# Performance work log

Hardware: AMD Instinct MI355X
Metric: run time of the kernel (lower is better)

## Reference

```python
import jax, jax.numpy as jnp
import numpy as np
import math

B, T, D, H = 4, 2048, 1024, 16
DH = D // H

def setup_inputs() -> dict:
    key = jax.random.key(0)
    ks = jax.random.split(key, 12)
    s = 1.0 / math.sqrt(D)
    inp = {
        'q': jax.random.normal(ks[0], (B, T, D), jnp.float32),
        'k': jax.random.normal(ks[1], (B, T, D), jnp.float32),
        'v': jax.random.normal(ks[2], (B, T, D), jnp.float32),
        # causal attn_mask [B, Tq, Tk]; all-keep padding mask [B,1,1,Tk]
        'attn_mask': jnp.broadcast_to(jnp.tril(jnp.ones((T, T), jnp.bool_)), (B, T, T)),
        'key_keep_mask': jnp.ones((B, 1, 1, T), jnp.bool_),
        'wq_w': jax.random.normal(ks[3], (D, D), jnp.float32) * s,
        'wq_b': jnp.zeros((D,), jnp.float32),
        'wk_w': jax.random.normal(ks[4], (D, D), jnp.float32) * s,
        'wk_b': jnp.zeros((D,), jnp.float32),
        'wv_w': jax.random.normal(ks[5], (D, D), jnp.float32) * s,
        'wv_b': jnp.zeros((D,), jnp.float32),
        'wo_w': jax.random.normal(ks[6], (D, D), jnp.float32) * s,
        'wo_b': jnp.zeros((D,), jnp.float32),
    }
    return inp

def reference(q, k, v, attn_mask, key_keep_mask, wq_w, wq_b, wk_w, wk_b, wv_w, wv_b, wo_w, wo_b):
    # projections (torch Linear: x @ W^T + b)
    Q = (q @ wq_w.T + wq_b).reshape(B, -1, H, DH).transpose(0, 2, 1, 3)  # [B,H,Tq,DH]
    K = (k @ wk_w.T + wk_b).reshape(B, -1, H, DH).transpose(0, 2, 1, 3)
    V = (v @ wv_w.T + wv_b).reshape(B, -1, H, DH).transpose(0, 2, 1, 3)
    scores = jnp.einsum('bhqd,bhkd->bhqk', Q, K) / math.sqrt(DH)
    neg_inf = jnp.array(-jnp.inf, scores.dtype)
    scores = jnp.where(attn_mask[:, None, :, :], scores, neg_inf)
    scores = jnp.where(key_keep_mask, scores, neg_inf)
    attn = jax.nn.softmax(scores, axis=-1)  # dropout p=0 -> identity
    out = jnp.einsum('bhqk,bhkd->bhqd', attn, V)
    out = out.transpose(0, 2, 1, 3).reshape(B, -1, D)
    return out @ wo_w.T + wo_b
```

## Files before the change

kernel.cpp:

```cpp
#include <hip/hip_runtime.h>
#include <cstdint>
#include <cstddef>


typedef float f32x4 __attribute__((ext_vector_type(4)));
typedef short bf16x8 __attribute__((ext_vector_type(8)));
typedef float fltx4 __attribute__((ext_vector_type(4)));
typedef unsigned short u16x4 __attribute__((ext_vector_type(4)));

#define GLOBAL_AS __attribute__((address_space(1)))
#define LDS_AS __attribute__((address_space(3)))

__device__ __forceinline__ unsigned short f2bf(float f) {
    union { float f; unsigned int u; } x;
    x.f = f;
    unsigned int u = x.u;
    unsigned int r = (u + 0x7FFFu + ((u >> 16) & 1u)) >> 16;
    return (unsigned short)r;
}

__device__ __forceinline__ unsigned int pack_trunc(float a, float b) {
    union { float f; unsigned int u; } x, y;
    x.f = a; y.f = b;
    return (x.u >> 16) | (y.u & 0xFFFF0000u);
}

__global__ __launch_bounds__(256) void cast_all_kernel(
    const float* __restrict__ q, const float* __restrict__ k, const float* __restrict__ v,
    const float* __restrict__ wq, const float* __restrict__ wk,
    const float* __restrict__ wv, const float* __restrict__ wo,
    unsigned short* __restrict__ dst)
{
    const size_t SEG = 8388608;
    const size_t WSEG = 1048576;
    size_t i = ((size_t)blockIdx.x * 256 + threadIdx.x) * 4;
    const float* src;
    size_t off;
    if (i < SEG)               { src = q;  off = i; }
    else if (i < 2 * SEG)      { src = k;  off = i - SEG; }
    else if (i < 3 * SEG)      { src = v;  off = i - 2 * SEG; }
    else if (i < 3 * SEG + WSEG)     { src = wq; off = i - 3 * SEG; }
    else if (i < 3 * SEG + 2 * WSEG) { src = wk; off = i - 3 * SEG - WSEG; }
    else if (i < 3 * SEG + 3 * WSEG) { src = wv; off = i - 3 * SEG - 2 * WSEG; }
    else                             { src = wo; off = i - 3 * SEG - 3 * WSEG; }
    fltx4 val = *(const fltx4*)(src + off);
    u16x4 o;
    o[0] = f2bf(val[0]);
    o[1] = f2bf(val[1]);
    o[2] = f2bf(val[2]);
    o[3] = f2bf(val[3]);
    *(u16x4*)(dst + i) = o;
}

__global__ __launch_bounds__(256) void qkv_gemm_kernel(
    const unsigned short* __restrict__ X,
    const unsigned short* __restrict__ Wc,
    const float* __restrict__ bq, const float* __restrict__ bk,
    const float* __restrict__ bv,
    unsigned short* __restrict__ Outs,
    float qscale)
{
    const int z = blockIdx.z;
    const unsigned short* A  = X  + (size_t)z * 8388608;
    const unsigned short* Bw = Wc + (size_t)z * 1048576;
    const float* bias = (z == 0) ? bq : (z == 1) ? bk : bv;
    unsigned short* outp = Outs + (size_t)z * 8388608;
    const float scale = (z == 0) ? qscale : 1.0f;
    const bool vmode = (z == 2);

    __shared__ __align__(16) unsigned short lA[128 * 32];
    __shared__ __align__(16) unsigned short lB[128 * 32];
    const int tid = threadIdx.x;
    const int w = tid >> 6, lane = tid & 63;
    const int quad = lane >> 4, l16 = lane & 15;

    const int lin = blockIdx.x + (blockIdx.y << 3);
    const int r_ = lin & 7, s_ = lin >> 3;
    const int bm = ((r_ << 3) | (s_ & 7)) * 128;
    const int bn = (s_ >> 3) * 128;

    const int wm = (w >> 1) * 64, wn = (w & 1) * 64;

    f32x4 acc[4][4] = {};
    const int srow0 = w * 16 + (lane >> 2);

    for (int kb = 0; kb < 32; ++kb) {
        const unsigned short* Ab = A + (size_t)bm * 1024 + kb * 32;
        const unsigned short* Bb = Bw + (size_t)bn * 1024 + kb * 32;
#pragma unroll
        for (int i = 0; i < 2; ++i) {
            int row = i * 64 + srow0;
            int gcb = (lane & 3) ^ ((row >> 1) & 3);
            __builtin_amdgcn_global_load_lds(
                (const GLOBAL_AS unsigned int*)(Ab + (size_t)row * 1024 + gcb * 8),
                (LDS_AS unsigned int*)(lA + i * 2048 + w * 512), 16, 0, 0);
            __builtin_amdgcn_global_load_lds(
                (const GLOBAL_AS unsigned int*)(Bb + (size_t)row * 1024 + gcb * 8),
                (LDS_AS unsigned int*)(lB + i * 2048 + w * 512), 16, 0, 0);
        }
        __syncthreads();

        bf16x8 af[4], bfr[4];
#pragma unroll
        for (int mi = 0; mi < 4; ++mi) {
            int row = wm + mi * 16 + l16;
            af[mi] = *(const bf16x8*)(lA + row * 32 + ((quad ^ ((row >> 1) & 3)) * 8));
        }
#pragma unroll
        for (int ni = 0; ni < 4; ++ni) {
            int row = wn + ni * 16 + l16;
            bfr[ni] = *(const bf16x8*)(lB + row * 32 + ((quad ^ ((row >> 1) & 3)) * 8));
        }
#pragma unroll
        for (int mi = 0; mi < 4; ++mi)
#pragma unroll
            for (int ni = 0; ni < 4; ++ni)
                acc[mi][ni] = __builtin_amdgcn_mfma_f32_16x16x32_bf16(af[mi], bfr[ni], acc[mi][ni], 0, 0, 0);
        __syncthreads();
    }

#pragma unroll
    for (int mi = 0; mi < 4; ++mi) {
        int rowb = bm + wm + mi * 16 + quad * 4;
#pragma unroll
        for (int ni = 0; ni < 4; ++ni) {
            int col = bn + wn + ni * 16 + l16;
            float bv_ = bias[col];
#pragma unroll
            for (int r = 0; r < 4; ++r) {
                int m = rowb + r;
                float vout = (acc[mi][ni][r] + bv_) * scale;
                int b = m >> 11, t = m & 2047, h = col >> 6, d = col & 63;
                if (!vmode) {
                    outp[((size_t)(b * 16 + h) * 2048 + t) * 64 + d] = f2bf(vout);
                } else {
                    outp[((size_t)(b * 16 + h) * 64 + d) * 2048 + t] = f2bf(vout);
                }
            }
        }
    }
}

__global__ __launch_bounds__(256) void out_gemm_kernel(
    const unsigned short* __restrict__ A,
    const unsigned short* __restrict__ Bw,
    const float* __restrict__ bias,
    float* __restrict__ outp)
{
    __shared__ __align__(16) unsigned short lA[128 * 32];
    __shared__ __align__(16) unsigned short lB[128 * 32];
    const int tid = threadIdx.x;
    const int w = tid >> 6, lane = tid & 63;
    const int quad = lane >> 4, l16 = lane & 15;

    const int lin = blockIdx.x + (blockIdx.y << 3);
    const int r_ = lin & 7, s_ = lin >> 3;
    const int bm = ((r_ << 3) | (s_ & 7)) * 128;
    const int bn = (s_ >> 3) * 128;

    const int wm = (w >> 1) * 64, wn = (w & 1) * 64;

    f32x4 acc[4][4] = {};
    const int srow0 = w * 16 + (lane >> 2);

    for (int kb = 0; kb < 32; ++kb) {
        const unsigned short* Ab = A + (size_t)bm * 1024 + kb * 32;
        const unsigned short* Bb = Bw + (size_t)bn * 1024 + kb * 32;
#pragma unroll
        for (int i = 0; i < 2; ++i) {
            int row = i * 64 + srow0;
            int gcb = (lane & 3) ^ ((row >> 1) & 3);
            __builtin_amdgcn_global_load_lds(
                (const GLOBAL_AS unsigned int*)(Ab + (size_t)row * 1024 + gcb * 8),
                (LDS_AS unsigned int*)(lA + i * 2048 + w * 512), 16, 0, 0);
            __builtin_amdgcn_global_load_lds(
                (const GLOBAL_AS unsigned int*)(Bb + (size_t)row * 1024 + gcb * 8),
                (LDS_AS unsigned int*)(lB + i * 2048 + w * 512), 16, 0, 0);
        }
        __syncthreads();

        bf16x8 af[4], bfr[4];
#pragma unroll
        for (int mi = 0; mi < 4; ++mi) {
            int row = wm + mi * 16 + l16;
            af[mi] = *(const bf16x8*)(lA + row * 32 + ((quad ^ ((row >> 1) & 3)) * 8));
        }
#pragma unroll
        for (int ni = 0; ni < 4; ++ni) {
            int row = wn + ni * 16 + l16;
            bfr[ni] = *(const bf16x8*)(lB + row * 32 + ((quad ^ ((row >> 1) & 3)) * 8));
        }
#pragma unroll
        for (int mi = 0; mi < 4; ++mi)
#pragma unroll
            for (int ni = 0; ni < 4; ++ni)
                acc[mi][ni] = __builtin_amdgcn_mfma_f32_16x16x32_bf16(af[mi], bfr[ni], acc[mi][ni], 0, 0, 0);
        __syncthreads();
    }

#pragma unroll
    for (int mi = 0; mi < 4; ++mi) {
        int rowb = bm + wm + mi * 16 + quad * 4;
#pragma unroll
        for (int ni = 0; ni < 4; ++ni) {
            int col = bn + wn + ni * 16 + l16;
            float bv_ = bias[col];
#pragma unroll
            for (int r = 0; r < 4; ++r)
                outp[(size_t)(rowb + r) * 1024 + col] = acc[mi][ni][r] + bv_;
        }
    }
}

__global__ __launch_bounds__(256) void attn_kernel(
    const unsigned short* __restrict__ Qh,
    const unsigned short* __restrict__ Kh,
    const unsigned short* __restrict__ Vt,
    unsigned short* __restrict__ att)
{
    const int tid = threadIdx.x;
    const int w = tid >> 6, lane = tid & 63;
    const int qd = lane >> 4, l16 = lane & 15;
    const int bh = blockIdx.x;
    const int pairy = blockIdx.y;

    const unsigned short* Qp = Qh + (size_t)bh * 2048 * 64;
    const unsigned short* Kp = Kh + (size_t)bh * 2048 * 64;
    const unsigned short* Vp = Vt + (size_t)bh * 64 * 2048;
    const int b = bh >> 4, h = bh & 15;

    __shared__ __align__(16) unsigned short Kl[2][64 * 64];
    __shared__ __align__(16) unsigned short Vl[2][64 * 64];
    __shared__ __align__(16) unsigned short Pl[4][2][16 * 64];

    auto stage = [&](int kt, int buf) {
#pragma unroll
        for (int j = 0; j < 2; ++j) {
            int r = w * 16 + j * 8 + (lane >> 3);
            int c = (lane & 7) ^ (r & 7);
            __builtin_amdgcn_global_load_lds(
                (const GLOBAL_AS unsigned int*)(Kp + (size_t)(kt * 64 + r) * 64 + c * 8),
                (LDS_AS unsigned int*)(&Kl[buf][(w * 16 + j * 8) * 64]), 16, 0, 0);
            __builtin_amdgcn_global_load_lds(
                (const GLOBAL_AS unsigned int*)(Vp + (size_t)r * 2048 + kt * 64 + c * 8),
                (LDS_AS unsigned int*)(&Vl[buf][(w * 16 + j * 8) * 64]), 16, 0, 0);
        }
    };

    auto run_phase = [&](int qblk) {
        const int wqbase = qblk * 128 + w * 32;
        const int ktmax = 2 * qblk + 1;

        bf16x8 qa[2][2];
#pragma unroll
        for (int qt = 0; qt < 2; ++qt)
#pragma unroll
            for (int ks = 0; ks < 2; ++ks)
                qa[qt][ks] = *(const bf16x8*)(Qp + (size_t)(wqbase + qt * 16 + l16) * 64 + ks * 32 + qd * 8);

        float lp[2] = {0.0f, 0.0f};
        f32x4 O[2][4] = {};

        __syncthreads();
        stage(0, 0);

        for (int kt = 0; kt <= ktmax; ++kt) {
            __syncthreads();
            if (kt < ktmax) stage(kt + 1, (kt + 1) & 1);

            if (kt * 64 <= wqbase + 31) {
                const unsigned short* kl = &Kl[kt & 1][0];
                const unsigned short* vl = &Vl[kt & 1][0];

                bf16x8 kf[4][2];
#pragma unroll
                for (int nt = 0; nt < 4; ++nt)
#pragma unroll
                    for (int ks = 0; ks < 2; ++ks)
                        kf[nt][ks] = *(const bf16x8*)(kl + (nt * 16 + l16) * 64 +
                                                      (((ks * 4 + qd) ^ (l16 & 7)) * 8));

                f32x4 S[2][4];
#pragma unroll
                for (int qt = 0; qt < 2; ++qt)
#pragma unroll
                    for (int nt = 0; nt < 4; ++nt) {
                        f32x4 a = {};
                        a = __builtin_amdgcn_mfma_f32_16x16x32_bf16(kf[nt][0], qa[qt][0], a, 0, 0, 0);
                        a = __builtin_amdgcn_mfma_f32_16x16x32_bf16(kf[nt][1], qa[qt][1], a, 0, 0, 0);
                        S[qt][nt] = a;
                    }

                if (kt * 64 + 63 > wqbase) {
#pragma unroll
                    for (int qt = 0; qt < 2; ++qt) {
                        int qrow = wqbase + qt * 16 + l16;
#pragma unroll
                        for (int nt = 0; nt < 4; ++nt) {
                            int kbase = kt * 64 + nt * 16 + qd * 4;
#pragma unroll
                            for (int r = 0; r < 4; ++r)
                                if (kbase + r > qrow) S[qt][nt][r] = -INFINITY;
                        }
                    }
                }

#pragma unroll
                for (int qt = 0; qt < 2; ++qt) {
                    float s0 = 0.0f;
#pragma unroll
                    for (int nt = 0; nt < 4; ++nt)
#pragma unroll
                        for (int r = 0; r < 4; ++r) {
                            float e = __builtin_amdgcn_exp2f(S[qt][nt][r]);
                            S[qt][nt][r] = e;
                            s0 += e;
                        }
                    lp[qt] += s0;
                }

#pragma unroll
                for (int qt = 0; qt < 2; ++qt) {
                    unsigned short* pw = &Pl[w][qt][0];
#pragma unroll
                    for (int nt = 0; nt < 4; ++nt) {
                        uint2 pv;
                        pv.x = pack_trunc(S[qt][nt][0], S[qt][nt][1]);
                        pv.y = pack_trunc(S[qt][nt][2], S[qt][nt][3]);
                        int chunk = (2 * nt + (qd >> 1)) ^ (l16 & 7);
                        *(uint2*)(pw + l16 * 64 + chunk * 8 + (qd & 1) * 4) = pv;
                    }
                }
                asm volatile("s_waitcnt lgkmcnt(0)" ::: "memory");

                bf16x8 pa[2][2];
#pragma unroll
                for (int qt = 0; qt < 2; ++qt)
#pragma unroll
                    for (int s = 0; s < 2; ++s)
                        pa[qt][s] = *(const bf16x8*)(&Pl[w][qt][0] + l16 * 64 +
                                                     (((s * 4 + qd) ^ (l16 & 7)) * 8));

                bf16x8 vf[2][4];
#pragma unroll
                for (int s = 0; s < 2; ++s)
#pragma unroll
                    for (int dh = 0; dh < 4; ++dh)
                        vf[s][dh] = *(const bf16x8*)(vl + (dh * 16 + l16) * 64 +
                                                     (((s * 4 + qd) ^ (l16 & 7)) * 8));
#pragma unroll
                for (int qt = 0; qt < 2; ++qt)
#pragma unroll
                    for (int dh = 0; dh < 4; ++dh) {
                        O[qt][dh] = __builtin_amdgcn_mfma_f32_16x16x32_bf16(pa[qt][0], vf[0][dh], O[qt][dh], 0, 0, 0);
                        O[qt][dh] = __builtin_amdgcn_mfma_f32_16x16x32_bf16(pa[qt][1], vf[1][dh], O[qt][dh], 0, 0, 0);
                    }
            }
        }

#pragma unroll
        for (int qt = 0; qt < 2; ++qt) {
            float lsum = lp[qt];
            lsum += __shfl_xor(lsum, 16, 64);
            lsum += __shfl_xor(lsum, 32, 64);
            float linv = 1.0f / lsum;
#pragma unroll
            for (int r = 0; r < 4; ++r) {
                float lC = __shfl(linv, qd * 4 + r, 64);
                int t = wqbase + qt * 16 + qd * 4 + r;
#pragma unroll
                for (int dh = 0; dh < 4; ++dh) {
                    size_t idx = (size_t)(b * 2048 + t) * 1024 + h * 64 + dh * 16 + l16;
                    att[idx] = f2bf(O[qt][dh][r] * lC);
                }
            }
        }
    };

    run_phase(15 - pairy);
    run_phase(pairy);
}

extern "C" void kernel_launch(void* const* d_in, const int* in_sizes, int n_in,
                              void* d_out, int out_size, void* d_ws, size_t ws_size,
                              hipStream_t stream)
{
    const float* q = (const float*)d_in[0];
    const float* k = (const float*)d_in[1];
    const float* v = (const float*)d_in[2];
    const float* wq_w = (const float*)d_in[5];
    const float* wq_b = (const float*)d_in[6];
    const float* wk_w = (const float*)d_in[7];
    const float* wk_b = (const float*)d_in[8];
    const float* wv_w = (const float*)d_in[9];
    const float* wv_b = (const float*)d_in[10];
    const float* wo_w = (const float*)d_in[11];
    const float* wo_b = (const float*)d_in[12];

    unsigned short* ws = (unsigned short*)d_ws;
    unsigned short* xq  = ws;
    unsigned short* wqc = ws + 25165824;
    unsigned short* woc = ws + 28311552;
    unsigned short* Qhp = ws + 29360128;
    unsigned short* Khp = ws + 37748736;
    unsigned short* Vtp = ws + 46137344;
    unsigned short* att = xq;

    (void)in_sizes; (void)n_in; (void)out_size; (void)ws_size;

    cast_all_kernel<<<28672, 256, 0, stream>>>(q, k, v, wq_w, wk_w, wv_w, wo_w, ws);

    qkv_gemm_kernel<<<dim3(8, 64, 3), 256, 0, stream>>>(
        xq, wqc, wq_b, wk_b, wv_b, Qhp, 0.1803368801f);

    attn_kernel<<<dim3(64, 8), 256, 0, stream>>>(Qhp, Khp, Vtp, att);

    out_gemm_kernel<<<dim3(8, 64), 256, 0, stream>>>(att, woc, wo_b, (float*)d_out);
}
```

Before: 361.0 us.

## Fuse activation fp32-to-bf16 cast into QKV GEMM and enlarge attention query tile

The separate cast pass over q/k/v is removed. The QKV GEMM now loads fp32 activations directly, rounds them to bf16 in registers and writes them to LDS, which saves a full write and re-read of 48 MB of bf16 intermediates. The attention kernel now gives each wave 64 query rows instead of 32 and launches half as many blocks, so each staged K/V tile is reused across more queries. The costs are synchronous fp32 loads in place of async global_load_lds for A, more registers in attention with occupancy limited to 1, and fewer blocks for load balancing.

Result: slower. 390.9 us (+8.3%).

```diff
diff --git a/kernel.cpp b/kernel.cpp
--- a/kernel.cpp
+++ b/kernel.cpp
@@ -25,24 +25,25 @@
     return (x.u >> 16) | (y.u & 0xFFFF0000u);
 }
 
-__global__ __launch_bounds__(256) void cast_all_kernel(
-    const float* __restrict__ q, const float* __restrict__ k, const float* __restrict__ v,
+__device__ __forceinline__ unsigned int pack_rh(float a, float b) {
+    union { float f; unsigned int u; } x, y;
+    x.f = a; y.f = b;
+    return ((x.u + 0x8000u) >> 16) | ((y.u + 0x8000u) & 0xFFFF0000u);
+}
+
+__global__ __launch_bounds__(256) void cast_w_kernel(
     const float* __restrict__ wq, const float* __restrict__ wk,
     const float* __restrict__ wv, const float* __restrict__ wo,
     unsigned short* __restrict__ dst)
 {
-    const size_t SEG = 8388608;
     const size_t WSEG = 1048576;
     size_t i = ((size_t)blockIdx.x * 256 + threadIdx.x) * 4;
     const float* src;
     size_t off;
-    if (i < SEG)               { src = q;  off = i; }
-    else if (i < 2 * SEG)      { src = k;  off = i - SEG; }
-    else if (i < 3 * SEG)      { src = v;  off = i - 2 * SEG; }
-    else if (i < 3 * SEG + WSEG)     { src = wq; off = i - 3 * SEG; }
-    else if (i < 3 * SEG + 2 * WSEG) { src = wk; off = i - 3 * SEG - WSEG; }
-    else if (i < 3 * SEG + 3 * WSEG) { src = wv; off = i - 3 * SEG - 2 * WSEG; }
-    else                             { src = wo; off = i - 3 * SEG - 3 * WSEG; }
+    if (i < WSEG)          { src = wq; off = i; }
+    else if (i < 2 * WSEG) { src = wk; off = i - WSEG; }
+    else if (i < 3 * WSEG) { src = wv; off = i - 2 * WSEG; }
+    else                   { src = wo; off = i - 3 * WSEG; }
     fltx4 val = *(const fltx4*)(src + off);
     u16x4 o;
     o[0] = f2bf(val[0]);
@@ -53,7 +54,8 @@
 }
 
 __global__ __launch_bounds__(256) void qkv_gemm_kernel(
-    const unsigned short* __restrict__ X,
+    const float* __restrict__ qx, const float* __restrict__ kx,
+    const float* __restrict__ vx,
     const unsigned short* __restrict__ Wc,
     const float* __restrict__ bq, const float* __restrict__ bk,
     const float* __restrict__ bv,
@@ -61,7 +63,7 @@
     float qscale)
 {
     const int z = blockIdx.z;
-    const unsigned short* A  = X  + (size_t)z * 8388608;
+    const float* A32 = (z == 0) ? qx : (z == 1) ? kx : vx;
     const unsigned short* Bw = Wc + (size_t)z * 1048576;
     const float* bias = (z == 0) ? bq : (z == 1) ? bk : bv;
     unsigned short* outp = Outs + (size_t)z * 8388608;
@@ -83,17 +85,23 @@
 
     f32x4 acc[4][4] = {};
     const int srow0 = w * 16 + (lane >> 2);
+    const int gc = lane & 3;
 
     for (int kb = 0; kb < 32; ++kb) {
-        const unsigned short* Ab = A + (size_t)bm * 1024 + kb * 32;
         const unsigned short* Bb = Bw + (size_t)bn * 1024 + kb * 32;
 #pragma unroll
         for (int i = 0; i < 2; ++i) {
             int row = i * 64 + srow0;
-            int gcb = (lane & 3) ^ ((row >> 1) & 3);
-            __builtin_amdgcn_global_load_lds(
-                (const GLOBAL_AS unsigned int*)(Ab + (size_t)row * 1024 + gcb * 8),
-                (LDS_AS unsigned int*)(lA + i * 2048 + w * 512), 16, 0, 0);
+            const float* src = A32 + (size_t)(bm + row) * 1024 + kb * 32 + gc * 8;
+            fltx4 v0 = *(const fltx4*)(src);
+            fltx4 v1 = *(const fltx4*)(src + 4);
+            uint4 pk;
+            pk.x = pack_rh(v0[0], v0[1]);
+            pk.y = pack_rh(v0[2], v0[3]);
+            pk.z = pack_rh(v1[0], v1[1]);
+            pk.w = pack_rh(v1[2], v1[3]);
+            *(uint4*)(lA + row * 32 + (gc ^ ((row >> 1) & 3)) * 8) = pk;
+            int gcb = gc ^ ((row >> 1) & 3);
             __builtin_amdgcn_global_load_lds(
                 (const GLOBAL_AS unsigned int*)(Bb + (size_t)row * 1024 + gcb * 8),
                 (LDS_AS unsigned int*)(lB + i * 2048 + w * 512), 16, 0, 0);
@@ -212,7 +220,7 @@
     }
 }
 
-__global__ __launch_bounds__(256) void attn_kernel(
+__global__ __launch_bounds__(256, 1) void attn_kernel(
     const unsigned short* __restrict__ Qh,
     const unsigned short* __restrict__ Kh,
     const unsigned short* __restrict__ Vt,
@@ -231,7 +239,7 @@
 
     __shared__ __align__(16) unsigned short Kl[2][64 * 64];
     __shared__ __align__(16) unsigned short Vl[2][64 * 64];
-    __shared__ __align__(16) unsigned short Pl[4][2][16 * 64];
+    __shared__ __align__(16) unsigned short Pl[4][4][16 * 64];
 
     auto stage = [&](int kt, int buf) {
 #pragma unroll
@@ -248,18 +256,18 @@
     };
 
     auto run_phase = [&](int qblk) {
-        const int wqbase = qblk * 128 + w * 32;
-        const int ktmax = 2 * qblk + 1;
-
-        bf16x8 qa[2][2];
-#pragma unroll
-        for (int qt = 0; qt < 2; ++qt)
+        const int wqbase = qblk * 256 + w * 64;
+        const int ktmax = 4 * qblk + 3;
+
+        bf16x8 qa[4][2];
+#pragma unroll
+        for (int qt = 0; qt < 4; ++qt)
 #pragma unroll
             for (int ks = 0; ks < 2; ++ks)
                 qa[qt][ks] = *(const bf16x8*)(Qp + (size_t)(wqbase + qt * 16 + l16) * 64 + ks * 32 + qd * 8);
 
-        float lp[2] = {0.0f, 0.0f};
-        f32x4 O[2][4] = {};
+        float lp[4] = {0.0f, 0.0f, 0.0f, 0.0f};
+        f32x4 O[4][4] = {};
 
         __syncthreads();
         stage(0, 0);
@@ -268,7 +276,7 @@
             __syncthreads();
             if (kt < ktmax) stage(kt + 1, (kt + 1) & 1);
 
-            if (kt * 64 <= wqbase + 31) {
+            if (kt * 64 <= wqbase + 63) {
                 const unsigned short* kl = &Kl[kt & 1][0];
                 const unsigned short* vl = &Vl[kt & 1][0];
 
@@ -280,9 +288,9 @@
                         kf[nt][ks] = *(const bf16x8*)(kl + (nt * 16 + l16) * 64 +
                                                       (((ks * 4 + qd) ^ (l16 & 7)) * 8));
 
-                f32x4 S[2][4];
-#pragma unroll
-                for (int qt = 0; qt < 2; ++qt)
+                f32x4 S[4][4];
+#pragma unroll
+                for (int qt = 0; qt < 4; ++qt)
 #pragma unroll
                     for (int nt = 0; nt < 4; ++nt) {
                         f32x4 a = {};
@@ -293,7 +301,7 @@
 
                 if (kt * 64 + 63 > wqbase) {
 #pragma unroll
-                    for (int qt = 0; qt < 2; ++qt) {
+                    for (int qt = 0; qt < 4; ++qt) {
                         int qrow = wqbase + qt * 16 + l16;
 #pragma unroll
                         for (int nt = 0; nt < 4; ++nt) {
@@ -306,7 +314,7 @@
                 }
 
 #pragma unroll
-                for (int qt = 0; qt < 2; ++qt) {
+                for (int qt = 0; qt < 4; ++qt) {
                     float s0 = 0.0f;
 #pragma unroll
                     for (int nt = 0; nt < 4; ++nt)
@@ -320,7 +328,7 @@
                 }
 
 #pragma unroll
-                for (int qt = 0; qt < 2; ++qt) {
+                for (int qt = 0; qt < 4; ++qt) {
                     unsigned short* pw = &Pl[w][qt][0];
 #pragma unroll
                     for (int nt = 0; nt < 4; ++nt) {
@@ -333,9 +341,9 @@
                 }
                 asm volatile("s_waitcnt lgkmcnt(0)" ::: "memory");
 
-                bf16x8 pa[2][2];
-#pragma unroll
-                for (int qt = 0; qt < 2; ++qt)
+                bf16x8 pa[4][2];
+#pragma unroll
+                for (int qt = 0; qt < 4; ++qt)
 #pragma unroll
                     for (int s = 0; s < 2; ++s)
                         pa[qt][s] = *(const bf16x8*)(&Pl[w][qt][0] + l16 * 64 +
@@ -349,7 +357,7 @@
                         vf[s][dh] = *(const bf16x8*)(vl + (dh * 16 + l16) * 64 +
                                                      (((s * 4 + qd) ^ (l16 & 7)) * 8));
 #pragma unroll
-                for (int qt = 0; qt < 2; ++qt)
+                for (int qt = 0; qt < 4; ++qt)
 #pragma unroll
                     for (int dh = 0; dh < 4; ++dh) {
                         O[qt][dh] = __builtin_amdgcn_mfma_f32_16x16x32_bf16(pa[qt][0], vf[0][dh], O[qt][dh], 0, 0, 0);
@@ -359,7 +367,7 @@
         }
 
 #pragma unroll
-        for (int qt = 0; qt < 2; ++qt) {
+        for (int qt = 0; qt < 4; ++qt) {
             float lsum = lp[qt];
             lsum += __shfl_xor(lsum, 16, 64);
             lsum += __shfl_xor(lsum, 32, 64);
@@ -377,7 +385,7 @@
         }
     };
 
-    run_phase(15 - pairy);
+    run_phase(7 - pairy);
     run_phase(pairy);
 }
 
@@ -398,22 +406,21 @@
     const float* wo_b = (const float*)d_in[12];
 
     unsigned short* ws = (unsigned short*)d_ws;
-    unsigned short* xq  = ws;
+    unsigned short* att = ws;
     unsigned short* wqc = ws + 25165824;
     unsigned short* woc = ws + 28311552;
     unsigned short* Qhp = ws + 29360128;
     unsigned short* Khp = ws + 37748736;
     unsigned short* Vtp = ws + 46137344;
-    unsigned short* att = xq;
 
     (void)in_sizes; (void)n_in; (void)out_size; (void)ws_size;
 
-    cast_all_kernel<<<28672, 256, 0, stream>>>(q, k, v, wq_w, wk_w, wv_w, wo_w, ws);
+    cast_w_kernel<<<4096, 256, 0, stream>>>(wq_w, wk_w, wv_w, wo_w, wqc);
 
     qkv_gemm_kernel<<<dim3(8, 64, 3), 256, 0, stream>>>(
-        xq, wqc, wq_b, wk_b, wv_b, Qhp, 0.1803368801f);
-
-    attn_kernel<<<dim3(64, 8), 256, 0, stream>>>(Qhp, Khp, Vtp, att);
+        q, k, v, wqc, wq_b, wk_b, wv_b, Qhp, 0.1803368801f);
+
+    attn_kernel<<<dim3(64, 4), 256, 0, stream>>>(Qhp, Khp, Vtp, att);
 
     out_gemm_kernel<<<dim3(8, 64), 256, 0, stream>>>(att, woc, wo_b, (float*)d_out);
 }
```
